# Optimization experiments

Measured on AMD Instinct MI355X. Metric: run time of the kernel, lower is better.

## Reference

```python
import jax, jax.numpy as jnp
import numpy as np
from jax.scipy.special import logsumexp

B, T, K = 256, 512, 128


def setup_inputs() -> dict:
    key = jax.random.key(0)
    k1, k2, k3, k4 = jax.random.split(key, 4)
    logits = jax.random.normal(k1, (B, T, K), dtype=jnp.float32)
    labels = jax.random.randint(k2, (B, T), 0, K)
    # lengths in [1, T] (a zero-length sequence is degenerate for a CRF)
    seq_lens = jax.random.randint(k3, (B,), 1, T + 1, dtype=jnp.int32)
    # tf.random.uniform default is U[0,1)
    trans_params = jax.random.uniform(k4, (K, K), dtype=jnp.float32)
    return {"logits": logits, "labels": labels, "seq_lens": seq_lens,
            "trans_params": trans_params}


def _viterbi_decode(logits, trans, seq_lens):
    # tfa.text.crf_decode: max-plus forward pass storing backpointers, then backtrace.
    b, t, k = logits.shape
    mask = jnp.arange(t)[None, :] < seq_lens[:, None]              # [B,T]
    alpha0 = logits[:, 0]                                           # [B,K]
    id_k = jnp.arange(k)[None, :]

    def fwd(alpha, xs):
        emit, m = xs                                                # [B,K], [B]
        scores = alpha[:, :, None] + trans[None]                    # [B,Kprev,Kcur]
        bp = jnp.where(m[:, None], jnp.argmax(scores, axis=1), id_k)
        alpha_new = jnp.where(m[:, None], jnp.max(scores, axis=1) + emit, alpha)
        return alpha_new, bp

    emits = jnp.swapaxes(logits[:, 1:], 0, 1)                       # [T-1,B,K]
    alpha_t, bps = jax.lax.scan(fwd, alpha0, (emits, mask[:, 1:].T))
    last = jnp.argmax(alpha_t, axis=1)                              # [B]

    def back(tag, bp):
        prev = jnp.take_along_axis(bp, tag[:, None], axis=1)[:, 0]
        return prev, prev

    _, tags_rev = jax.lax.scan(back, last, bps, reverse=True)       # [T-1,B]
    return jnp.concatenate([tags_rev, last[None, :]], axis=0).T     # [B,T]


def _crf_log_norm(logits, trans, seq_lens):
    # forward algorithm in log space, frozen past each sequence's length
    b, t, k = logits.shape
    mask = jnp.arange(t)[None, :] < seq_lens[:, None]

    def fwd(alpha, xs):
        emit, m = xs
        new = logsumexp(alpha[:, :, None] + trans[None], axis=1) + emit
        return jnp.where(m[:, None], new, alpha), None

    emits = jnp.swapaxes(logits[:, 1:], 0, 1)
    alpha_t, _ = jax.lax.scan(fwd, logits[:, 0], (emits, mask[:, 1:].T))
    return logsumexp(alpha_t, axis=1)                               # [B]


def _crf_sequence_score(logits, labels, trans, seq_lens):
    b, t, k = logits.shape
    mask = (jnp.arange(t)[None, :] < seq_lens[:, None]).astype(logits.dtype)
    unary = jnp.sum(jnp.take_along_axis(logits, labels[..., None], axis=2)[..., 0] * mask, axis=1)
    tmask = (jnp.arange(1, t)[None, :] < seq_lens[:, None]).astype(logits.dtype)
    binary = jnp.sum(trans[labels[:, :-1], labels[:, 1:]] * tmask, axis=1)
    return unary + binary                                           # [B]


def reference(logits, labels, seq_lens, trans_params):
    pred_ids = _viterbi_decode(logits, trans_params, seq_lens)
    log_likelihood = (_crf_sequence_score(logits, labels, trans_params, seq_lens)
                      - _crf_log_norm(logits, trans_params, seq_lens))
    loss = jnp.sum(-log_likelihood)
    return loss, pred_ids
```

## Files before the change

kernel.cpp:

```cpp
#include <hip/hip_runtime.h>
#include <math.h>

#define BB 256
#define TT 512
#define KK 128
#define AIDX(i) ((i) + (((i) >> 5) << 2))

typedef float v2f __attribute__((ext_vector_type(2)));
typedef unsigned short u16v2 __attribute__((ext_vector_type(2)));

template<int CTRL>
__device__ __forceinline__ int dpp_i(int x) {
  return __builtin_amdgcn_update_dpp(x, x, CTRL, 0xF, 0xF, true);
}
template<int CTRL>
__device__ __forceinline__ float dpp_f(float x) {
  return __int_as_float(dpp_i<CTRL>(__float_as_int(x)));
}
__device__ __forceinline__ float swz16_f(float x) {
  return __int_as_float(__builtin_amdgcn_ds_swizzle(__float_as_int(x), 0x401F));
}
__device__ __forceinline__ int pkminu16(int a, int b) {
  u16v2 av = *(u16v2*)&a, bv = *(u16v2*)&b;
  u16v2 r = __builtin_elementwise_min(av, bv);
  return *(int*)&r;
}
#define BARRIER_LGKM() asm volatile("s_waitcnt lgkmcnt(0)\ns_barrier" ::: "memory")

__global__ __launch_bounds__(512, 4) void crf_fwd(
    const float* __restrict__ logits,
    const int* __restrict__ labels,
    const int* __restrict__ seq_lens,
    const float* __restrict__ trans,
    float* __restrict__ negll,
    int* __restrict__ lastIdx,
    float* __restrict__ mOut)
{
  const int tid = threadIdx.x;
  const int cg = tid >> 3, rg = tid & 7;
  const int j0 = cg * 2, i0 = rg * 16;

  if (blockIdx.x < BB) {
    const int b = blockIdx.x;
    const int L = seq_lens[b];
    __shared__ __align__(16) float av[2][144];
    __shared__ float rv[8]; __shared__ int ri[8];

    v2f tv[16];
#pragma unroll
    for (int ii = 0; ii < 16; ++ii)
      tv[ii] = *(const v2f*)&trans[(i0 + ii) * KK + j0];

    if (tid < KK) av[0][AIDX(tid)] = logits[(b * TT) * KK + tid];

    v2f emC[4], emN[4];
#pragma unroll
    for (int s = 0; s < 4; ++s) {
      int t2 = 1 + s; if (t2 > L - 1) t2 = (L > 1) ? (L - 1) : 0;
      emC[s] = *(const v2f*)&logits[(b * TT + t2) * KK + j0];
    }
    __syncthreads();

    for (int tc = 1; tc < L; tc += 4) {
#pragma unroll
      for (int s = 0; s < 4; ++s) {
        int t2 = tc + 4 + s; if (t2 > L - 1) t2 = L - 1;
        emN[s] = *(const v2f*)&logits[(b * TT + t2) * KK + j0];
      }
#pragma unroll
      for (int s = 0; s < 4; ++s) {
        const int t = tc + s;
        if (t >= L) break;
        const float4* avr = (const float4*)(av[(t & 1) ^ 1] + AIDX(i0));
        v2f sv[16];
#pragma unroll
        for (int q = 0; q < 4; ++q) {
          float4 a4 = avr[q];
#pragma unroll
          for (int c = 0; c < 4; ++c) {
            float a = (c == 0) ? a4.x : (c == 1) ? a4.y : (c == 2) ? a4.z : a4.w;
            sv[q * 4 + c] = (v2f){a, a} + tv[q * 4 + c];
          }
        }
        v2f m;
        {
          v2f m0 = __builtin_elementwise_max(sv[0], sv[1]);
          v2f m1 = __builtin_elementwise_max(sv[2], sv[3]);
          v2f m2 = __builtin_elementwise_max(sv[4], sv[5]);
          v2f m3 = __builtin_elementwise_max(sv[6], sv[7]);
          v2f m4 = __builtin_elementwise_max(sv[8], sv[9]);
          v2f m5 = __builtin_elementwise_max(sv[10], sv[11]);
          v2f m6 = __builtin_elementwise_max(sv[12], sv[13]);
          v2f m7 = __builtin_elementwise_max(sv[14], sv[15]);
          m0 = __builtin_elementwise_max(m0, m1);
          m2 = __builtin_elementwise_max(m2, m3);
          m4 = __builtin_elementwise_max(m4, m5);
          m6 = __builtin_elementwise_max(m6, m7);
          m0 = __builtin_elementwise_max(m0, m2);
          m4 = __builtin_elementwise_max(m4, m6);
          m = __builtin_elementwise_max(m0, m4);
        }
        {
          v2f o;
          o.x = dpp_f<0xB1>(m.x); o.y = dpp_f<0xB1>(m.y);
          m = __builtin_elementwise_max(m, o);
          o.x = dpp_f<0x4E>(m.x); o.y = dpp_f<0x4E>(m.y);
          m = __builtin_elementwise_max(m, o);
          o.x = dpp_f<0x141>(m.x); o.y = dpp_f<0x141>(m.y);
          m = __builtin_elementwise_max(m, o);
        }
        v2f nav = m + emC[s];
        if (rg == 0) {
          *(v2f*)(av[t & 1] + AIDX(j0)) = nav;
          *(v2f*)&mOut[(b * TT + t) * KK + j0] = m;
        }
        BARRIER_LGKM();
      }
#pragma unroll
      for (int s = 0; s < 4; ++s) emC[s] = emN[s];
    }

    const float* avf = av[(L - 1) & 1];
    {
      float v = (tid < KK) ? avf[AIDX(tid)] : -3.4e38f;
      int idx = (tid < KK) ? tid : KK;
#pragma unroll
      for (int mm = 1; mm < 64; mm <<= 1) {
        float ov = __shfl_xor(v, mm);
        int oi = __shfl_xor(idx, mm);
        if (ov > v || (ov == v && oi < idx)) { v = ov; idx = oi; }
      }
      if ((tid & 63) == 0) { rv[tid >> 6] = v; ri[tid >> 6] = idx; }
    }
    __syncthreads();
    if (tid == 0) {
      float bv = rv[0]; int bi = ri[0];
#pragma unroll
      for (int w = 1; w < 8; ++w)
        if (rv[w] > bv || (rv[w] == bv && ri[w] < bi)) { bv = rv[w]; bi = ri[w]; }
      lastIdx[b] = bi;
    }

  } else {
    const int b = blockIdx.x - BB;
    const int L = seq_lens[b];
    __shared__ __align__(16) float ev[2][144];
    __shared__ __align__(16) float wmax[16];
    __shared__ float rs[8]; __shared__ float rsc[8];

    v2f tw[16];
#pragma unroll
    for (int ii = 0; ii < 16; ++ii) {
      v2f tr = *(const v2f*)&trans[(i0 + ii) * KK + j0];
      tw[ii].x = __expf(tr.x);
      tw[ii].y = __expf(tr.y);
    }
    if (tid < KK) ev[0][AIDX(tid)] = __expf(logits[(b * TT) * KK + tid]);
    if (tid < 16) wmax[tid] = 1.0f;

    v2f emC[4], emN[4];
#pragma unroll
    for (int s = 0; s < 4; ++s) {
      int t2 = 1 + s; if (t2 > L - 1) t2 = (L > 1) ? (L - 1) : 0;
      emC[s] = *(const v2f*)&logits[(b * TT + t2) * KK + j0];
    }
    __syncthreads();

    float Cln = 0.0f;
    for (int tc = 1; tc < L; tc += 4) {
#pragma unroll
      for (int s = 0; s < 4; ++s) {
        int t2 = tc + 4 + s; if (t2 > L - 1) t2 = L - 1;
        emN[s] = *(const v2f*)&logits[(b * TT + t2) * KK + j0];
      }
      float r;
      {
        float4 w0 = *(const float4*)&wmax[0];
        float4 w1 = *(const float4*)&wmax[4];
        float4 w2 = *(const float4*)&wmax[8];
        float4 w3 = *(const float4*)&wmax[12];
        float U = fmaxf(fmaxf(fmaxf(w0.x, w0.y), fmaxf(w0.z, w0.w)),
                        fmaxf(fmaxf(w1.x, w1.y), fmaxf(w1.z, w1.w)));
        U = fmaxf(U, fmaxf(fmaxf(fmaxf(w2.x, w2.y), fmaxf(w2.z, w2.w)),
                           fmaxf(fmaxf(w3.x, w3.y), fmaxf(w3.z, w3.w))));
        int ex = (__float_as_int(U) >> 23) & 255;
        r = __int_as_float((254 - ex) << 23);
        Cln += (float)(ex - 127) * 0.6931471805599453f;
      }
#pragma unroll
      for (int s = 0; s < 4; ++s) {
        const int t = tc + s;
        if (t >= L) break;
        const float4* evr = (const float4*)(ev[(t & 1) ^ 1] + AIDX(i0));
        v2f S2 = {0.0f, 0.0f};
#pragma unroll
        for (int q = 0; q < 4; ++q) {
          float4 e4 = evr[q];
#pragma unroll
          for (int c = 0; c < 4; ++c) {
            float e = (c == 0) ? e4.x : (c == 1) ? e4.y : (c == 2) ? e4.z : e4.w;
            S2 += (v2f){e, e} * tw[q * 4 + c];
          }
        }
        {
          v2f o;
          o.x = dpp_f<0xB1>(S2.x); o.y = dpp_f<0xB1>(S2.y); S2 += o;
          o.x = dpp_f<0x4E>(S2.x); o.y = dpp_f<0x4E>(S2.y); S2 += o;
          o.x = dpp_f<0x141>(S2.x); o.y = dpp_f<0x141>(S2.y); S2 += o;
        }
        v2f em2 = emC[s];
        float evn0 = S2.x * __expf(em2.x);
        float evn1 = S2.y * __expf(em2.y);
        if (s == 0) { evn0 *= r; evn1 *= r; }
        if (rg == 0)
          *(v2f*)(ev[t & 1] + AIDX(j0)) = (v2f){evn0, evn1};
        if (s == 3) {
          float wm = fmaxf(evn0, evn1);
          wm = fmaxf(wm, dpp_f<0x140>(wm));
          wm = fmaxf(wm, swz16_f(wm));
          if ((tid & 31) == 0) wmax[tid >> 5] = wm;
        }
        BARRIER_LGKM();
      }
#pragma unroll
      for (int s = 0; s < 4; ++s) emC[s] = emN[s];
    }

    const float* evf = ev[(L - 1) & 1];
    {
      float ssum = (tid < KK) ? evf[AIDX(tid)] : 0.0f;
#pragma unroll
      for (int mm = 1; mm < 64; mm <<= 1) ssum += __shfl_xor(ssum, mm);
      if ((tid & 63) == 0) rs[tid >> 6] = ssum;
    }
    float sc = 0.0f;
    for (int tt2 = tid; tt2 < L; tt2 += 512) {
      int lab = labels[b * TT + tt2];
      sc += logits[(b * TT + tt2) * KK + lab];
      if (tt2 >= 1) sc += trans[labels[b * TT + tt2 - 1] * KK + lab];
    }
#pragma unroll
    for (int mm = 1; mm < 64; mm <<= 1) sc += __shfl_xor(sc, mm);
    if ((tid & 63) == 0) rsc[tid >> 6] = sc;
    __syncthreads();
    if (tid == 0) {
      float es = rs[0]; float scf = rsc[0];
#pragma unroll
      for (int w = 1; w < 8; ++w) { es += rs[w]; scf += rsc[w]; }
      negll[b] = (Cln + logf(es)) - scf;
    }
  }
}

__global__ __launch_bounds__(64, 1) void crf_backtrack(
    const float* __restrict__ mvec,
    const float* __restrict__ logits,
    const int* __restrict__ seq_lens,
    const int* __restrict__ lastIdx,
    const float* __restrict__ trans,
    float* __restrict__ pred_out)
{
  const int b = blockIdx.x, l = threadIdx.x;
  const int L = seq_lens[b];
  __shared__ float tT[KK][KK + 2];
  __shared__ float tagsf[TT];

  for (int i = 0; i < KK; ++i) {
    v2f r = *(const v2f*)&trans[i * KK + 2 * l];
    tT[2 * l][i] = r.x;
    tT[2 * l + 1][i] = r.y;
  }
  const int last = lastIdx[b];
  for (int t = l; t < TT; t += 64) tagsf[t] = (float)last;
  __syncthreads();

  if (L >= 2) {
    const float* mb = mvec   + (size_t)(b * TT) * KK + 2 * l;
    const float* gb = logits + (size_t)(b * TT) * KK + 2 * l;
    int tag = last;
    v2f mvC = *(const v2f*)&mb[(size_t)(L - 1) * KK];

    v2f lg0, lg1, lg2, lg3, lg4, lg5, lg6, lg7;
    v2f mv0, mv1, mv2, mv3, mv4, mv5, mv6, mv7;
#define INITLD(P) { int s_ = L - 2 - (P); int sc_ = s_ < 0 ? 0 : s_;            \
      lg##P = *(const v2f*)&gb[(size_t)sc_ * KK];                              \
      mv##P = *(const v2f*)&mb[(size_t)sc_ * KK]; }
    INITLD(0) INITLD(1) INITLD(2) INITLD(3)
    INITLD(4) INITLD(5) INITLD(6) INITLD(7)
#undef INITLD

    int t = L - 1;

#define STEP_BODY(LG, MV, GUARDED)                                             \
    {                                                                          \
      const int tp = t - 1;                                                    \
      v2f aP;                                                                  \
      if (GUARDED) aP = (tp >= 1) ? (MV + LG) : LG;                            \
      else         aP = MV + LG;                                               \
      int lanem = tag >> 1;                                                    \
      int txi = __builtin_amdgcn_readlane(__float_as_int(mvC.x), lanem);       \
      int tyi = __builtin_amdgcn_readlane(__float_as_int(mvC.y), lanem);       \
      float target = __int_as_float((tag & 1) ? tyi : txi);                    \
      v2f col = *(const v2f*)&tT[tag][2 * l];                                  \
      v2f sv = aP + col;                           \
      bool h0 = (sv.x == target), h1 = (sv.y == target);                       \
      unsigned long long mask = __ballot(h0 || h1);                            \
      int first = __ffsll(mask) - 1;                 \
      int cand = h0 ? (2 * l) : (2 * l + 1);                                   \
      tag = __builtin_amdgcn_readlane(cand, first);                            \
      if (l == 0) tagsf[tp] = (float)tag;                                      \
      mvC = MV;                                                                \
    }

    while (t >= 9) {
#define MAIN_PHASE(P)                                                          \
      STEP_BODY(lg##P, mv##P, false)                                           \
      { int sN = t - 9; int sc_ = sN < 0 ? 0 : sN;                             \
        lg##P = *(const v2f*)&gb[(size_t)sc_ * KK];                            \
        mv##P = *(const v2f*)&mb[(size_t)sc_ * KK]; }                          \
      --t;
      MAIN_PHASE(0) MAIN_PHASE(1) MAIN_PHASE(2) MAIN_PHASE(3)
      MAIN_PHASE(4) MAIN_PHASE(5) MAIN_PHASE(6) MAIN_PHASE(7)
#undef MAIN_PHASE
    }

    while (t >= 1) {
      const int tp = t - 1;
      int sc_ = tp < 1 ? 0 : tp;
      v2f lgE = *(const v2f*)&gb[(size_t)tp * KK];
      v2f mvE = *(const v2f*)&mb[(size_t)sc_ * KK];
      STEP_BODY(lgE, mvE, true)
      --t;
    }
#undef STEP_BODY
  }
  __syncthreads();
#pragma unroll
  for (int k = 0; k < 8; ++k)
    pred_out[b * TT + l * 8 + k] = tagsf[l * 8 + k];
}

__global__ __launch_bounds__(512, 4) void crf_main_fb(
    const float* __restrict__ logits,
    const int* __restrict__ labels,
    const int* __restrict__ seq_lens,
    const float* __restrict__ trans,
    float* __restrict__ pred_out,
    float* __restrict__ negll,
    unsigned char* __restrict__ bp)
{
  const int tid = threadIdx.x;
  const int cg = tid >> 3, rg = tid & 7;
  const int j0 = cg * 2, i0 = rg * 16;

  if (blockIdx.x < BB) {
    const int b = blockIdx.x;
    const int L = seq_lens[b];
    __shared__ __align__(16) float av[2][144];
    __shared__ unsigned char tags[TT];
    __shared__ float rv[8]; __shared__ int ri[8];
    __shared__ int last_s;

    v2f tv[16];
#pragma unroll
    for (int ii = 0; ii < 16; ++ii)
      tv[ii] = *(const v2f*)&trans[(i0 + ii) * KK + j0];

    if (tid < KK) av[0][AIDX(tid)] = logits[(b * TT) * KK + tid];

    v2f emC[4], emN[4];
#pragma unroll
    for (int s = 0; s < 4; ++s) {
      int t2 = 1 + s; if (t2 > L - 1) t2 = (L > 1) ? (L - 1) : 0;
      emC[s] = *(const v2f*)&logits[(b * TT + t2) * KK + j0];
    }
    __syncthreads();

    unsigned int pw0 = 0, pw1 = 0; int pend_c = -1;

    for (int tc = 1; tc < L; tc += 4) {
#pragma unroll
      for (int s = 0; s < 4; ++s) {
        int t2 = tc + 4 + s; if (t2 > L - 1) t2 = L - 1;
        emN[s] = *(const v2f*)&logits[(b * TT + t2) * KK + j0];
      }
      if (pend_c >= 0 && rg == 1) {
        *(uint2*)(bp + (((b << 7) + pend_c) << 9) + (cg << 3)) =
            make_uint2(pw0, pw1);
      }
      unsigned int w0 = 0, w1 = 0;
#pragma unroll
      for (int s = 0; s < 4; ++s) {
        const int t = tc + s;
        if (t >= L) break;
        const float4* avr = (const float4*)(av[(t & 1) ^ 1] + AIDX(i0));
        v2f sv[16];
#pragma unroll
        for (int q = 0; q < 4; ++q) {
          float4 a4 = avr[q];
#pragma unroll
          for (int c = 0; c < 4; ++c) {
            float a = (c == 0) ? a4.x : (c == 1) ? a4.y : (c == 2) ? a4.z : a4.w;
            sv[q * 4 + c] = (v2f){a, a} + tv[q * 4 + c];
          }
        }
        v2f m;
        {
          v2f m0 = __builtin_elementwise_max(sv[0], sv[1]);
          v2f m1 = __builtin_elementwise_max(sv[2], sv[3]);
          v2f m2 = __builtin_elementwise_max(sv[4], sv[5]);
          v2f m3 = __builtin_elementwise_max(sv[6], sv[7]);
          v2f m4 = __builtin_elementwise_max(sv[8], sv[9]);
          v2f m5 = __builtin_elementwise_max(sv[10], sv[11]);
          v2f m6 = __builtin_elementwise_max(sv[12], sv[13]);
          v2f m7 = __builtin_elementwise_max(sv[14], sv[15]);
          m0 = __builtin_elementwise_max(m0, m1);
          m2 = __builtin_elementwise_max(m2, m3);
          m4 = __builtin_elementwise_max(m4, m5);
          m6 = __builtin_elementwise_max(m6, m7);
          m0 = __builtin_elementwise_max(m0, m2);
          m4 = __builtin_elementwise_max(m4, m6);
          m = __builtin_elementwise_max(m0, m4);
        }
        {
          v2f o;
          o.x = dpp_f<0xB1>(m.x); o.y = dpp_f<0xB1>(m.y);
          m = __builtin_elementwise_max(m, o);
          o.x = dpp_f<0x4E>(m.x); o.y = dpp_f<0x4E>(m.y);
          m = __builtin_elementwise_max(m, o);
          o.x = dpp_f<0x141>(m.x); o.y = dpp_f<0x141>(m.y);
          m = __builtin_elementwise_max(m, o);
        }
        int ai0 = 0xFFFF, ai1 = 0xFFFF;
#pragma unroll
        for (int i = 15; i >= 0; --i) {
          ai0 = (sv[i].x == m.x) ? (i0 + i) : ai0;
          ai1 = (sv[i].y == m.y) ? (i0 + i) : ai1;
        }
        int aip = ai0 | (ai1 << 16);
        aip = pkminu16(aip, dpp_i<0xB1>(aip));
        aip = pkminu16(aip, dpp_i<0x4E>(aip));
        aip = pkminu16(aip, dpp_i<0x141>(aip));

        v2f em2 = emC[s];
        if (rg == 0)
          *(v2f*)(av[t & 1] + AIDX(j0)) = m + em2;
        unsigned int pk = ((unsigned int)aip & 0xFFu) |
                          (((unsigned int)aip >> 8) & 0xFF00u);
        unsigned int sh = pk << ((s & 1) * 16);
        if (s < 2) w0 |= sh; else w1 |= sh;
        BARRIER_LGKM();
      }
      pw0 = w0; pw1 = w1; pend_c = (tc - 1) >> 2;
#pragma unroll
      for (int s = 0; s < 4; ++s) emC[s] = emN[s];
    }
    if (pend_c >= 0 && rg == 1) {
      *(uint2*)(bp + (((b << 7) + pend_c) << 9) + (cg << 3)) =
          make_uint2(pw0, pw1);
    }

    const float* avf = av[(L - 1) & 1];
    {
      float v = (tid < KK) ? avf[AIDX(tid)] : -3.4e38f;
      int idx = (tid < KK) ? tid : KK;
#pragma unroll
      for (int mm = 1; mm < 64; mm <<= 1) {
        float ov = __shfl_xor(v, mm);
        int oi = __shfl_xor(idx, mm);
        if (ov > v || (ov == v && oi < idx)) { v = ov; idx = oi; }
      }
      if ((tid & 63) == 0) { rv[tid >> 6] = v; ri[tid >> 6] = idx; }
    }
    __syncthreads();
    if (tid == 0) {
      float bv = rv[0]; int bi = ri[0];
#pragma unroll
      for (int w = 1; w < 8; ++w)
        if (rv[w] > bv || (rv[w] == bv && ri[w] < bi)) { bv = rv[w]; bi = ri[w]; }
      last_s = bi;
    }
    __syncthreads();
    const int last = last_s;
    if (tid >= L - 1 && tid < TT) tags[tid] = (unsigned char)last;
    __syncthreads();

    if (tid < 64 && L >= 2) {
      const uint2* bpv = (const uint2*)bp;
      int tag = last;
      int cTop = (L - 2) >> 2;
      uint2 q = bpv[(((b << 7) + cTop) << 6) + tid];
      for (int c = cTop; c >= 0; --c) {
        uint2 qn;
        if (c > 0) qn = bpv[(((b << 7) + (c - 1)) << 6) + tid];
        int sHi = (L - 2) - 4 * c; if (sHi > 3) sHi = 3;
#pragma unroll
        for (int s = 3; s >= 0; --s) {
          if (s <= sHi) {
            int word = (s < 2) ? (int)q.x : (int)q.y;
            unsigned int w = (unsigned int)__shfl(word, tag >> 1);
            tag = (int)((w >> ((((s & 1) << 1) | (tag & 1)) << 3)) & 255u);
            if (tid == 0) tags[4 * c + s] = (unsigned char)tag;
          }
        }
        q = qn;
      }
    }
    __syncthreads();
    pred_out[b * TT + tid] = (float)tags[tid];

  } else {
    const int b = blockIdx.x - BB;
    const int L = seq_lens[b];
    __shared__ __align__(16) float ev[2][144];
    __shared__ __align__(16) float wmax[16];
    __shared__ float rs[8]; __shared__ float rsc[8];

    v2f tw[16];
#pragma unroll
    for (int ii = 0; ii < 16; ++ii) {
      v2f tr = *(const v2f*)&trans[(i0 + ii) * KK + j0];
      tw[ii].x = __expf(tr.x);
      tw[ii].y = __expf(tr.y);
    }
    if (tid < KK) ev[0][AIDX(tid)] = __expf(logits[(b * TT) * KK + tid]);
    if (tid < 16) wmax[tid] = 1.0f;

    v2f emC[4], emN[4];
#pragma unroll
    for (int s = 0; s < 4; ++s) {
      int t2 = 1 + s; if (t2 > L - 1) t2 = (L > 1) ? (L - 1) : 0;
      emC[s] = *(const v2f*)&logits[(b * TT + t2) * KK + j0];
    }
    __syncthreads();

    float Cln = 0.0f;
    for (int tc = 1; tc < L; tc += 4) {
#pragma unroll
      for (int s = 0; s < 4; ++s) {
        int t2 = tc + 4 + s; if (t2 > L - 1) t2 = L - 1;
        emN[s] = *(const v2f*)&logits[(b * TT + t2) * KK + j0];
      }
      float r;
      {
        float4 w0 = *(const float4*)&wmax[0];
        float4 w1 = *(const float4*)&wmax[4];
        float4 w2 = *(const float4*)&wmax[8];
        float4 w3 = *(const float4*)&wmax[12];
        float U = fmaxf(fmaxf(fmaxf(w0.x, w0.y), fmaxf(w0.z, w0.w)),
                        fmaxf(fmaxf(w1.x, w1.y), fmaxf(w1.z, w1.w)));
        U = fmaxf(U, fmaxf(fmaxf(fmaxf(w2.x, w2.y), fmaxf(w2.z, w2.w)),
                           fmaxf(fmaxf(w3.x, w3.y), fmaxf(w3.z, w3.w))));
        int ex = (__float_as_int(U) >> 23) & 255;
        r = __int_as_float((254 - ex) << 23);
        Cln += (float)(ex - 127) * 0.6931471805599453f;
      }
#pragma unroll
      for (int s = 0; s < 4; ++s) {
        const int t = tc + s;
        if (t >= L) break;
        const float4* evr = (const float4*)(ev[(t & 1) ^ 1] + AIDX(i0));
        v2f S2 = {0.0f, 0.0f};
#pragma unroll
        for (int q = 0; q < 4; ++q) {
          float4 e4 = evr[q];
#pragma unroll
          for (int c = 0; c < 4; ++c) {
            float e = (c == 0) ? e4.x : (c == 1) ? e4.y : (c == 2) ? e4.z : e4.w;
            S2 += (v2f){e, e} * tw[q * 4 + c];
          }
        }
        {
          v2f o;
          o.x = dpp_f<0xB1>(S2.x); o.y = dpp_f<0xB1>(S2.y); S2 += o;
          o.x = dpp_f<0x4E>(S2.x); o.y = dpp_f<0x4E>(S2.y); S2 += o;
          o.x = dpp_f<0x141>(S2.x); o.y = dpp_f<0x141>(S2.y); S2 += o;
        }
        v2f em2 = emC[s];
        float evn0 = S2.x * __expf(em2.x);
        float evn1 = S2.y * __expf(em2.y);
        if (s == 0) { evn0 *= r; evn1 *= r; }
        if (rg == 0)
          *(v2f*)(ev[t & 1] + AIDX(j0)) = (v2f){evn0, evn1};
        if (s == 3) {
          float wm = fmaxf(evn0, evn1);
          wm = fmaxf(wm, dpp_f<0x140>(wm));
          wm = fmaxf(wm, swz16_f(wm));
          if ((tid & 31) == 0) wmax[tid >> 5] = wm;
        }
        BARRIER_LGKM();
      }
#pragma unroll
      for (int s = 0; s < 4; ++s) emC[s] = emN[s];
    }

    const float* evf = ev[(L - 1) & 1];
    {
      float ssum = (tid < KK) ? evf[AIDX(tid)] : 0.0f;
#pragma unroll
      for (int mm = 1; mm < 64; mm <<= 1) ssum += __shfl_xor(ssum, mm);
      if ((tid & 63) == 0) rs[tid >> 6] = ssum;
    }
    float sc = 0.0f;
    for (int tt2 = tid; tt2 < L; tt2 += 512) {
      int lab = labels[b * TT + tt2];
      sc += logits[(b * TT + tt2) * KK + lab];
      if (tt2 >= 1) sc += trans[labels[b * TT + tt2 - 1] * KK + lab];
    }
#pragma unroll
    for (int mm = 1; mm < 64; mm <<= 1) sc += __shfl_xor(sc, mm);
    if ((tid & 63) == 0) rsc[tid >> 6] = sc;
    __syncthreads();
    if (tid == 0) {
      float es = rs[0]; float scf = rsc[0];
#pragma unroll
      for (int w = 1; w < 8; ++w) { es += rs[w]; scf += rsc[w]; }
      negll[b] = (Cln + logf(es)) - scf;
    }
  }
}

__global__ void crf_loss_reduce(const float* __restrict__ negll, float* __restrict__ out) {
  int tid = threadIdx.x;
  float v = negll[tid];
#pragma unroll
  for (int m = 1; m < 64; m <<= 1) v += __shfl_xor(v, m);
  __shared__ float p[4];
  if ((tid & 63) == 0) p[tid >> 6] = v;
  __syncthreads();
  if (tid == 0) out[0] = p[0] + p[1] + p[2] + p[3];
}

extern "C" void kernel_launch(void* const* d_in, const int* in_sizes, int n_in,
                              void* d_out, int out_size, void* d_ws, size_t ws_size,
                              hipStream_t stream) {
  const float* logits   = (const float*)d_in[0];
  const int*   labels   = (const int*)d_in[1];
  const int*   seq_lens = (const int*)d_in[2];
  const float* trans    = (const float*)d_in[3];
  float* out = (float*)d_out;

  float* negll = (float*)d_ws;
  const size_t M_OFF = 4096;
  const size_t NEED = M_OFF + (size_t)BB * TT * KK * 4;

  if (ws_size >= NEED) {
    int*   lastIdx = (int*)((char*)d_ws + 1024);
    float* mOut    = (float*)((char*)d_ws + M_OFF);
    crf_fwd<<<2 * BB, 512, 0, stream>>>(logits, labels, seq_lens, trans,
                                        negll, lastIdx, mOut);
    crf_backtrack<<<BB, 64, 0, stream>>>(mOut, logits, seq_lens, lastIdx,
                                         trans, out + 1);
  } else {
    unsigned char* bp = (unsigned char*)d_ws + 1024;
    crf_main_fb<<<2 * BB, 512, 0, stream>>>(logits, labels, seq_lens, trans,
                                            out + 1, negll, bp);
  }
  crf_loss_reduce<<<1, 256, 0, stream>>>(negll, out);
}
```

Baseline: 435.3 us.

## Fuse Viterbi backtrack into the forward kernel's Viterbi blocks

The separate backtrack kernel is removed. Each Viterbi block of the forward kernel now runs the backtrace itself with one wavefront, after staging the transposed transition matrix and a tag buffer in a shared-memory arena that is carved up by offsets. This removes a kernel launch and its serialization, and lets backtraces for short sequences overlap with the log-norm blocks still running. The cost is more LDS per block (about 70KB), which can limit how many blocks fit per CU, and 448 idle threads sitting in each block during the serial backtrace.

```diff
diff --git a/kernel.cpp b/kernel.cpp
--- a/kernel.cpp
+++ b/kernel.cpp
@@ -6,6 +6,17 @@
 #define KK 128
 #define AIDX(i) ((i) + (((i) >> 5) << 2))
 
+#define SM_TT    0
+#define SM_AV    16640
+#define SM_TAGS  16928
+#define SM_RV    17440
+#define SM_RI    17448
+#define SM_LAST  17456
+#define SM_WMAX  17460
+#define SM_RS    17476
+#define SM_RSC   17484
+#define SM_TOTAL 17496
+
 typedef float v2f __attribute__((ext_vector_type(2)));
 typedef unsigned short u16v2 __attribute__((ext_vector_type(2)));
 
@@ -27,15 +38,16 @@
 }
 #define BARRIER_LGKM() asm volatile("s_waitcnt lgkmcnt(0)\ns_barrier" ::: "memory")
 
-__global__ __launch_bounds__(512, 4) void crf_fwd(
+__global__ __launch_bounds__(512, 4) void crf_main(
     const float* __restrict__ logits,
     const int* __restrict__ labels,
     const int* __restrict__ seq_lens,
     const float* __restrict__ trans,
+    float* __restrict__ pred_out,
     float* __restrict__ negll,
-    int* __restrict__ lastIdx,
     float* __restrict__ mOut)
 {
+  __shared__ __align__(16) float smem[SM_TOTAL];
   const int tid = threadIdx.x;
   const int cg = tid >> 3, rg = tid & 7;
   const int j0 = cg * 2, i0 = rg * 16;
@@ -43,8 +55,17 @@
   if (blockIdx.x < BB) {
     const int b = blockIdx.x;
     const int L = seq_lens[b];
-    __shared__ __align__(16) float av[2][144];
-    __shared__ float rv[8]; __shared__ int ri[8];
+    float* tT    = smem + SM_TT;
+    float (*av)[144] = (float(*)[144])(smem + SM_AV);
+    float* tagsf = smem + SM_TAGS;
+    float* rv    = smem + SM_RV;
+    int*   ri    = (int*)(smem + SM_RI);
+    int*   last_s = (int*)(smem + SM_LAST);
+
+    for (int e = tid; e < KK * KK; e += 512) {
+      int i = e >> 7, j = e & 127;
+      tT[j * 130 + i] = trans[e];
+    }
 
     v2f tv[16];
 #pragma unroll
@@ -138,15 +159,87 @@
 #pragma unroll
       for (int w = 1; w < 8; ++w)
         if (rv[w] > bv || (rv[w] == bv && ri[w] < bi)) { bv = rv[w]; bi = ri[w]; }
-      lastIdx[b] = bi;
-    }
+      *last_s = bi;
+    }
+    __syncthreads();
+    const int last = *last_s;
+    for (int t = tid; t < TT; t += 512) tagsf[t] = (float)last;
+    __syncthreads();
+
+    if (tid >= 64) return;
+    const int l = tid;
+
+    if (L >= 2) {
+      const float* mb = mOut   + (size_t)(b * TT) * KK + 2 * l;
+      const float* gb = logits + (size_t)(b * TT) * KK + 2 * l;
+      int tag = last;
+      v2f mvC = *(const v2f*)&mb[(size_t)(L - 1) * KK];
+
+      v2f lg0, lg1, lg2, lg3, lg4, lg5, lg6, lg7;
+      v2f mv0, mv1, mv2, mv3, mv4, mv5, mv6, mv7;
+#define INITLD(P) { int s_ = L - 2 - (P); int sc_ = s_ < 0 ? 0 : s_;           \
+      lg##P = *(const v2f*)&gb[(size_t)sc_ * KK];                              \
+      mv##P = *(const v2f*)&mb[(size_t)sc_ * KK]; }
+      INITLD(0) INITLD(1) INITLD(2) INITLD(3)
+      INITLD(4) INITLD(5) INITLD(6) INITLD(7)
+#undef INITLD
+
+      int t = L - 1;
+
+#define STEP_BODY(LG, MV, GUARDED)                                             \
+      {                                                                        \
+        const int tp = t - 1;                                                  \
+        v2f aP;                                                                \
+        if (GUARDED) aP = (tp >= 1) ? (MV + LG) : LG;                          \
+        else         aP = MV + LG;                                             \
+        int lanem = tag >> 1;                                                  \
+        int txi = __builtin_amdgcn_readlane(__float_as_int(mvC.x), lanem);     \
+        int tyi = __builtin_amdgcn_readlane(__float_as_int(mvC.y), lanem);     \
+        float target = __int_as_float((tag & 1) ? tyi : txi);                  \
+        v2f col = *(const v2f*)&tT[tag * 130 + 2 * l];                         \
+        v2f sv = aP + col;                         \
+        bool h0 = (sv.x == target), h1 = (sv.y == target);                     \
+        unsigned long long mask = __ballot(h0 || h1);                          \
+        int first = __ffsll(mask) - 1;               \
+        int cand = h0 ? (2 * l) : (2 * l + 1);                                 \
+        tag = __builtin_amdgcn_readlane(cand, first);                          \
+        if (l == 0) tagsf[tp] = (float)tag;                                    \
+        mvC = MV;                                                              \
+      }
+
+      while (t >= 9) {
+#define MAIN_PHASE(P)                                                          \
+        STEP_BODY(lg##P, mv##P, false)                                         \
+        { int sN = t - 9; int sc_ = sN < 0 ? 0 : sN;                           \
+          lg##P = *(const v2f*)&gb[(size_t)sc_ * KK];                          \
+          mv##P = *(const v2f*)&mb[(size_t)sc_ * KK]; }                        \
+        --t;
+        MAIN_PHASE(0) MAIN_PHASE(1) MAIN_PHASE(2) MAIN_PHASE(3)
+        MAIN_PHASE(4) MAIN_PHASE(5) MAIN_PHASE(6) MAIN_PHASE(7)
+#undef MAIN_PHASE
+      }
+
+      while (t >= 1) {
+        const int tp = t - 1;
+        int sc_ = tp < 1 ? 0 : tp;
+        v2f lgE = *(const v2f*)&gb[(size_t)tp * KK];
+        v2f mvE = *(const v2f*)&mb[(size_t)sc_ * KK];
+        STEP_BODY(lgE, mvE, true)
+        --t;
+      }
+#undef STEP_BODY
+    }
+#pragma unroll
+    for (int k = 0; k < 8; ++k)
+      pred_out[b * TT + l * 8 + k] = tagsf[l * 8 + k];
 
   } else {
     const int b = blockIdx.x - BB;
     const int L = seq_lens[b];
-    __shared__ __align__(16) float ev[2][144];
-    __shared__ __align__(16) float wmax[16];
-    __shared__ float rs[8]; __shared__ float rsc[8];
+    float (*ev)[144] = (float(*)[144])(smem + SM_AV);
+    float* wmax = smem + SM_WMAX;
+    float* rs   = smem + SM_RS;
+    float* rsc  = smem + SM_RSC;
 
     v2f tw[16];
 #pragma unroll
@@ -250,94 +343,6 @@
       negll[b] = (Cln + logf(es)) - scf;
     }
   }
-}
-
-__global__ __launch_bounds__(64, 1) void crf_backtrack(
-    const float* __restrict__ mvec,
-    const float* __restrict__ logits,
-    const int* __restrict__ seq_lens,
-    const int* __restrict__ lastIdx,
-    const float* __restrict__ trans,
-    float* __restrict__ pred_out)
-{
-  const int b = blockIdx.x, l = threadIdx.x;
-  const int L = seq_lens[b];
-  __shared__ float tT[KK][KK + 2];
-  __shared__ float tagsf[TT];
-
-  for (int i = 0; i < KK; ++i) {
-    v2f r = *(const v2f*)&trans[i * KK + 2 * l];
-    tT[2 * l][i] = r.x;
-    tT[2 * l + 1][i] = r.y;
-  }
-  const int last = lastIdx[b];
-  for (int t = l; t < TT; t += 64) tagsf[t] = (float)last;
-  __syncthreads();
-
-  if (L >= 2) {
-    const float* mb = mvec   + (size_t)(b * TT) * KK + 2 * l;
-    const float* gb = logits + (size_t)(b * TT) * KK + 2 * l;
-    int tag = last;
-    v2f mvC = *(const v2f*)&mb[(size_t)(L - 1) * KK];
-
-    v2f lg0, lg1, lg2, lg3, lg4, lg5, lg6, lg7;
-    v2f mv0, mv1, mv2, mv3, mv4, mv5, mv6, mv7;
-#define INITLD(P) { int s_ = L - 2 - (P); int sc_ = s_ < 0 ? 0 : s_;            \
-      lg##P = *(const v2f*)&gb[(size_t)sc_ * KK];                              \
-      mv##P = *(const v2f*)&mb[(size_t)sc_ * KK]; }
-    INITLD(0) INITLD(1) INITLD(2) INITLD(3)
-    INITLD(4) INITLD(5) INITLD(6) INITLD(7)
-#undef INITLD
-
-    int t = L - 1;
-
-#define STEP_BODY(LG, MV, GUARDED)                                             \
-    {                                                                          \
-      const int tp = t - 1;                                                    \
-      v2f aP;                                                                  \
-      if (GUARDED) aP = (tp >= 1) ? (MV + LG) : LG;                            \
-      else         aP = MV + LG;                                               \
-      int lanem = tag >> 1;                                                    \
-      int txi = __builtin_amdgcn_readlane(__float_as_int(mvC.x), lanem);       \
-      int tyi = __builtin_amdgcn_readlane(__float_as_int(mvC.y), lanem);       \
-      float target = __int_as_float((tag & 1) ? tyi : txi);                    \
-      v2f col = *(const v2f*)&tT[tag][2 * l];                                  \
-      v2f sv = aP + col;                           \
-      bool h0 = (sv.x == target), h1 = (sv.y == target);                       \
-      unsigned long long mask = __ballot(h0 || h1);                            \
-      int first = __ffsll(mask) - 1;                 \
-      int cand = h0 ? (2 * l) : (2 * l + 1);                                   \
-      tag = __builtin_amdgcn_readlane(cand, first);                            \
-      if (l == 0) tagsf[tp] = (float)tag;                                      \
-      mvC = MV;                                                                \
-    }
-
-    while (t >= 9) {
-#define MAIN_PHASE(P)                                                          \
-      STEP_BODY(lg##P, mv##P, false)                                           \
-      { int sN = t - 9; int sc_ = sN < 0 ? 0 : sN;                             \
-        lg##P = *(const v2f*)&gb[(size_t)sc_ * KK];                            \
-        mv##P = *(const v2f*)&mb[(size_t)sc_ * KK]; }                          \
-      --t;
-      MAIN_PHASE(0) MAIN_PHASE(1) MAIN_PHASE(2) MAIN_PHASE(3)
-      MAIN_PHASE(4) MAIN_PHASE(5) MAIN_PHASE(6) MAIN_PHASE(7)
-#undef MAIN_PHASE
-    }
-
-    while (t >= 1) {
-      const int tp = t - 1;
-      int sc_ = tp < 1 ? 0 : tp;
-      v2f lgE = *(const v2f*)&gb[(size_t)tp * KK];
-      v2f mvE = *(const v2f*)&mb[(size_t)sc_ * KK];
-      STEP_BODY(lgE, mvE, true)
-      --t;
-    }
-#undef STEP_BODY
-  }
-  __syncthreads();
-#pragma unroll
-  for (int k = 0; k < 8; ++k)
-    pred_out[b * TT + l * 8 + k] = tagsf[l * 8 + k];
 }
 
 __global__ __launch_bounds__(512, 4) void crf_main_fb(
@@ -645,12 +650,9 @@
   const size_t NEED = M_OFF + (size_t)BB * TT * KK * 4;
 
   if (ws_size >= NEED) {
-    int*   lastIdx = (int*)((char*)d_ws + 1024);
-    float* mOut    = (float*)((char*)d_ws + M_OFF);
-    crf_fwd<<<2 * BB, 512, 0, stream>>>(logits, labels, seq_lens, trans,
-                                        negll, lastIdx, mOut);
-    crf_backtrack<<<BB, 64, 0, stream>>>(mOut, logits, seq_lens, lastIdx,
-                                         trans, out + 1);
+    float* mOut = (float*)((char*)d_ws + M_OFF);
+    crf_main<<<2 * BB, 512, 0, stream>>>(logits, labels, seq_lens, trans,
+                                         out + 1, negll, mOut);
   } else {
     unsigned char* bp = (unsigned char*)d_ws + 1024;
     crf_main_fb<<<2 * BB, 512, 0, stream>>>(logits, labels, seq_lens, trans,
```

After: 379.4 us, median of 2. 1.15x faster.

## Merge Viterbi, forward-algorithm and backtrack into one 1024-thread block per sequence

Applied to the files above, without the earlier changes.

Fuses the two-kernel path (a forward kernel with separate Viterbi and log-norm blocks, then a backtrack kernel) into a single kernel. Each block of 1024 threads handles one sequence: the first 512 threads run the Viterbi max-plus recursion and the other 512 run the scaled forward algorithm, sharing barriers. The block then does the backtrack in its first wavefront using a transposed trans matrix in LDS. This removes a kernel launch and the global round-trip of lastIdx, but couples the two recursions to one barrier schedule. It also leaves most of the 1024-thread block idle during the serial backtrack, which reduces how much backtrack work can overlap with other blocks' recursions.

```diff
diff --git a/kernel.cpp b/kernel.cpp
--- a/kernel.cpp
+++ b/kernel.cpp
@@ -6,6 +6,18 @@
 #define KK 128
 #define AIDX(i) ((i) + (((i) >> 5) << 2))
 
+#define SM_TT    0
+#define SM_AV    16640
+#define SM_EV    16928
+#define SM_TAGS  17216
+#define SM_WMAX  17728
+#define SM_RV    17744
+#define SM_RI    17752
+#define SM_RS    17760
+#define SM_RSC   17768
+#define SM_LAST  17776
+#define SM_TOTAL 17780
+
 typedef float v2f __attribute__((ext_vector_type(2)));
 typedef unsigned short u16v2 __attribute__((ext_vector_type(2)));
 
@@ -27,50 +39,90 @@
 }
 #define BARRIER_LGKM() asm volatile("s_waitcnt lgkmcnt(0)\ns_barrier" ::: "memory")
 
-__global__ __launch_bounds__(512, 4) void crf_fwd(
+__global__ __launch_bounds__(1024, 4) void crf_merged(
     const float* __restrict__ logits,
     const int* __restrict__ labels,
     const int* __restrict__ seq_lens,
     const float* __restrict__ trans,
+    float* __restrict__ pred_out,
     float* __restrict__ negll,
-    int* __restrict__ lastIdx,
     float* __restrict__ mOut)
 {
+  __shared__ __align__(16) float smem[SM_TOTAL];
   const int tid = threadIdx.x;
-  const int cg = tid >> 3, rg = tid & 7;
+  const bool isV = tid < 512;
+  const int ht = isV ? tid : tid - 512;
+  const int cg = ht >> 3, rg = ht & 7;
   const int j0 = cg * 2, i0 = rg * 16;
-
-  if (blockIdx.x < BB) {
-    const int b = blockIdx.x;
-    const int L = seq_lens[b];
-    __shared__ __align__(16) float av[2][144];
-    __shared__ float rv[8]; __shared__ int ri[8];
-
-    v2f tv[16];
+  const int b = blockIdx.x;
+  const int L = seq_lens[b];
+
+  float* tT    = smem + SM_TT;
+  float (*av)[144] = (float(*)[144])(smem + SM_AV);
+  float (*ev)[144] = (float(*)[144])(smem + SM_EV);
+  float* tagsf = smem + SM_TAGS;
+  float* wmax  = smem + SM_WMAX;
+  float* rv    = smem + SM_RV;
+  int*   ri    = (int*)(smem + SM_RI);
+  float* rs    = smem + SM_RS;
+  float* rsc   = smem + SM_RSC;
+  int*   last_s = (int*)(smem + SM_LAST);
+
+  v2f tA[16];
+  if (isV) {
+    for (int e = ht; e < KK * KK; e += 512) {
+      int i = e >> 7, j = e & 127;
+      tT[j * 130 + i] = trans[e];
+    }
 #pragma unroll
     for (int ii = 0; ii < 16; ++ii)
-      tv[ii] = *(const v2f*)&trans[(i0 + ii) * KK + j0];
-
-    if (tid < KK) av[0][AIDX(tid)] = logits[(b * TT) * KK + tid];
-
-    v2f emC[4], emN[4];
+      tA[ii] = *(const v2f*)&trans[(i0 + ii) * KK + j0];
+    if (ht < KK) av[0][AIDX(ht)] = logits[(b * TT) * KK + ht];
+  } else {
+#pragma unroll
+    for (int ii = 0; ii < 16; ++ii) {
+      v2f tr = *(const v2f*)&trans[(i0 + ii) * KK + j0];
+      tA[ii].x = __expf(tr.x);
+      tA[ii].y = __expf(tr.y);
+    }
+    if (ht < KK) ev[0][AIDX(ht)] = __expf(logits[(b * TT) * KK + ht]);
+    if (ht < 16) wmax[ht] = 1.0f;
+  }
+
+  v2f emC[4], emN[4];
+#pragma unroll
+  for (int s = 0; s < 4; ++s) {
+    int t2 = 1 + s; if (t2 > L - 1) t2 = (L > 1) ? (L - 1) : 0;
+    emC[s] = *(const v2f*)&logits[(b * TT + t2) * KK + j0];
+  }
+  __syncthreads();
+
+  float Cln = 0.0f;
+  for (int tc = 1; tc < L; tc += 4) {
 #pragma unroll
     for (int s = 0; s < 4; ++s) {
-      int t2 = 1 + s; if (t2 > L - 1) t2 = (L > 1) ? (L - 1) : 0;
-      emC[s] = *(const v2f*)&logits[(b * TT + t2) * KK + j0];
-    }
-    __syncthreads();
-
-    for (int tc = 1; tc < L; tc += 4) {
-#pragma unroll
-      for (int s = 0; s < 4; ++s) {
-        int t2 = tc + 4 + s; if (t2 > L - 1) t2 = L - 1;
-        emN[s] = *(const v2f*)&logits[(b * TT + t2) * KK + j0];
-      }
-#pragma unroll
-      for (int s = 0; s < 4; ++s) {
-        const int t = tc + s;
-        if (t >= L) break;
+      int t2 = tc + 4 + s; if (t2 > L - 1) t2 = L - 1;
+      emN[s] = *(const v2f*)&logits[(b * TT + t2) * KK + j0];
+    }
+    float r = 0.0f;
+    if (!isV) {
+      float4 w0 = *(const float4*)&wmax[0];
+      float4 w1 = *(const float4*)&wmax[4];
+      float4 w2 = *(const float4*)&wmax[8];
+      float4 w3 = *(const float4*)&wmax[12];
+      float U = fmaxf(fmaxf(fmaxf(w0.x, w0.y), fmaxf(w0.z, w0.w)),
+                      fmaxf(fmaxf(w1.x, w1.y), fmaxf(w1.z, w1.w)));
+      U = fmaxf(U, fmaxf(fmaxf(fmaxf(w2.x, w2.y), fmaxf(w2.z, w2.w)),
+                         fmaxf(fmaxf(w3.x, w3.y), fmaxf(w3.z, w3.w))));
+      int ex = (__float_as_int(U) >> 23) & 255;
+      r = __int_as_float((254 - ex) << 23);
+      Cln += (float)(ex - 127) * 0.6931471805599453f;
+    }
+#pragma unroll
+    for (int s = 0; s < 4; ++s) {
+      const int t = tc + s;
+      if (t >= L) break;
+      if (isV) {
         const float4* avr = (const float4*)(av[(t & 1) ^ 1] + AIDX(i0));
         v2f sv[16];
 #pragma unroll
@@ -79,7 +131,7 @@
 #pragma unroll
           for (int c = 0; c < 4; ++c) {
             float a = (c == 0) ? a4.x : (c == 1) ? a4.y : (c == 2) ? a4.z : a4.w;
-            sv[q * 4 + c] = (v2f){a, a} + tv[q * 4 + c];
+            sv[q * 4 + c] = (v2f){a, a} + tA[q * 4 + c];
           }
         }
         v2f m;
@@ -114,83 +166,7 @@
           *(v2f*)(av[t & 1] + AIDX(j0)) = nav;
           *(v2f*)&mOut[(b * TT + t) * KK + j0] = m;
         }
-        BARRIER_LGKM();
-      }
-#pragma unroll
-      for (int s = 0; s < 4; ++s) emC[s] = emN[s];
-    }
-
-    const float* avf = av[(L - 1) & 1];
-    {
-      float v = (tid < KK) ? avf[AIDX(tid)] : -3.4e38f;
-      int idx = (tid < KK) ? tid : KK;
-#pragma unroll
-      for (int mm = 1; mm < 64; mm <<= 1) {
-        float ov = __shfl_xor(v, mm);
-        int oi = __shfl_xor(idx, mm);
-        if (ov > v || (ov == v && oi < idx)) { v = ov; idx = oi; }
-      }
-      if ((tid & 63) == 0) { rv[tid >> 6] = v; ri[tid >> 6] = idx; }
-    }
-    __syncthreads();
-    if (tid == 0) {
-      float bv = rv[0]; int bi = ri[0];
-#pragma unroll
-      for (int w = 1; w < 8; ++w)
-        if (rv[w] > bv || (rv[w] == bv && ri[w] < bi)) { bv = rv[w]; bi = ri[w]; }
-      lastIdx[b] = bi;
-    }
-
-  } else {
-    const int b = blockIdx.x - BB;
-    const int L = seq_lens[b];
-    __shared__ __align__(16) float ev[2][144];
-    __shared__ __align__(16) float wmax[16];
-    __shared__ float rs[8]; __shared__ float rsc[8];
-
-    v2f tw[16];
-#pragma unroll
-    for (int ii = 0; ii < 16; ++ii) {
-      v2f tr = *(const v2f*)&trans[(i0 + ii) * KK + j0];
-      tw[ii].x = __expf(tr.x);
-      tw[ii].y = __expf(tr.y);
-    }
-    if (tid < KK) ev[0][AIDX(tid)] = __expf(logits[(b * TT) * KK + tid]);
-    if (tid < 16) wmax[tid] = 1.0f;
-
-    v2f emC[4], emN[4];
-#pragma unroll
-    for (int s = 0; s < 4; ++s) {
-      int t2 = 1 + s; if (t2 > L - 1) t2 = (L > 1) ? (L - 1) : 0;
-      emC[s] = *(const v2f*)&logits[(b * TT + t2) * KK + j0];
-    }
-    __syncthreads();
-
-    float Cln = 0.0f;
-    for (int tc = 1; tc < L; tc += 4) {
-#pragma unroll
-      for (int s = 0; s < 4; ++s) {
-        int t2 = tc + 4 + s; if (t2 > L - 1) t2 = L - 1;
-        emN[s] = *(const v2f*)&logits[(b * TT + t2) * KK + j0];
-      }
-      float r;
-      {
-        float4 w0 = *(const float4*)&wmax[0];
-        float4 w1 = *(const float4*)&wmax[4];
-        float4 w2 = *(const float4*)&wmax[8];
-        float4 w3 = *(const float4*)&wmax[12];
-        float U = fmaxf(fmaxf(fmaxf(w0.x, w0.y), fmaxf(w0.z, w0.w)),
-                        fmaxf(fmaxf(w1.x, w1.y), fmaxf(w1.z, w1.w)));
-        U = fmaxf(U, fmaxf(fmaxf(fmaxf(w2.x, w2.y), fmaxf(w2.z, w2.w)),
-                           fmaxf(fmaxf(w3.x, w3.y), fmaxf(w3.z, w3.w))));
-        int ex = (__float_as_int(U) >> 23) & 255;
-        r = __int_as_float((254 - ex) << 23);
-        Cln += (float)(ex - 127) * 0.6931471805599453f;
-      }
-#pragma unroll
-      for (int s = 0; s < 4; ++s) {
-        const int t = tc + s;
-        if (t >= L) break;
+      } else {
         const float4* evr = (const float4*)(ev[(t & 1) ^ 1] + AIDX(i0));
         v2f S2 = {0.0f, 0.0f};
 #pragma unroll
@@ -199,7 +175,7 @@
 #pragma unroll
           for (int c = 0; c < 4; ++c) {
             float e = (c == 0) ? e4.x : (c == 1) ? e4.y : (c == 2) ? e4.z : e4.w;
-            S2 += (v2f){e, e} * tw[q * 4 + c];
+            S2 += (v2f){e, e} * tA[q * 4 + c];
           }
         }
         {
@@ -218,73 +194,75 @@
           float wm = fmaxf(evn0, evn1);
           wm = fmaxf(wm, dpp_f<0x140>(wm));
           wm = fmaxf(wm, swz16_f(wm));
-          if ((tid & 31) == 0) wmax[tid >> 5] = wm;
-        }
-        BARRIER_LGKM();
-      }
-#pragma unroll
-      for (int s = 0; s < 4; ++s) emC[s] = emN[s];
-    }
-
+          if ((ht & 31) == 0) wmax[ht >> 5] = wm;
+        }
+      }
+      BARRIER_LGKM();
+    }
+#pragma unroll
+    for (int s = 0; s < 4; ++s) emC[s] = emN[s];
+  }
+
+  if (isV) {
+    const float* avf = av[(L - 1) & 1];
+    float v = (ht < KK) ? avf[AIDX(ht)] : -3.4e38f;
+    int idx = (ht < KK) ? ht : KK;
+#pragma unroll
+    for (int mm = 1; mm < 64; mm <<= 1) {
+      float ov = __shfl_xor(v, mm);
+      int oi = __shfl_xor(idx, mm);
+      if (ov > v || (ov == v && oi < idx)) { v = ov; idx = oi; }
+    }
+    if ((ht & 63) == 0) { rv[ht >> 6] = v; ri[ht >> 6] = idx; }
+  } else {
     const float* evf = ev[(L - 1) & 1];
-    {
-      float ssum = (tid < KK) ? evf[AIDX(tid)] : 0.0f;
-#pragma unroll
-      for (int mm = 1; mm < 64; mm <<= 1) ssum += __shfl_xor(ssum, mm);
-      if ((tid & 63) == 0) rs[tid >> 6] = ssum;
-    }
+    float ssum = (ht < KK) ? evf[AIDX(ht)] : 0.0f;
+#pragma unroll
+    for (int mm = 1; mm < 64; mm <<= 1) ssum += __shfl_xor(ssum, mm);
+    if ((ht & 63) == 0) rs[ht >> 6] = ssum;
     float sc = 0.0f;
-    for (int tt2 = tid; tt2 < L; tt2 += 512) {
+    for (int tt2 = ht; tt2 < L; tt2 += 512) {
       int lab = labels[b * TT + tt2];
       sc += logits[(b * TT + tt2) * KK + lab];
       if (tt2 >= 1) sc += trans[labels[b * TT + tt2 - 1] * KK + lab];
     }
 #pragma unroll
     for (int mm = 1; mm < 64; mm <<= 1) sc += __shfl_xor(sc, mm);
-    if ((tid & 63) == 0) rsc[tid >> 6] = sc;
-    __syncthreads();
-    if (tid == 0) {
-      float es = rs[0]; float scf = rsc[0];
-#pragma unroll
-      for (int w = 1; w < 8; ++w) { es += rs[w]; scf += rsc[w]; }
-      negll[b] = (Cln + logf(es)) - scf;
-    }
-  }
-}
-
-__global__ __launch_bounds__(64, 1) void crf_backtrack(
-    const float* __restrict__ mvec,
-    const float* __restrict__ logits,
-    const int* __restrict__ seq_lens,
-    const int* __restrict__ lastIdx,
-    const float* __restrict__ trans,
-    float* __restrict__ pred_out)
-{
-  const int b = blockIdx.x, l = threadIdx.x;
-  const int L = seq_lens[b];
-  __shared__ float tT[KK][KK + 2];
-  __shared__ float tagsf[TT];
-
-  for (int i = 0; i < KK; ++i) {
-    v2f r = *(const v2f*)&trans[i * KK + 2 * l];
-    tT[2 * l][i] = r.x;
-    tT[2 * l + 1][i] = r.y;
-  }
-  const int last = lastIdx[b];
-  for (int t = l; t < TT; t += 64) tagsf[t] = (float)last;
+    if ((ht & 63) == 0) rsc[ht >> 6] = sc;
+  }
   __syncthreads();
+  if (tid == 0) {
+    float bv = rv[0]; int bi = ri[0];
+#pragma unroll
+    for (int w = 1; w < 8; ++w)
+      if (rv[w] > bv || (rv[w] == bv && ri[w] < bi)) { bv = rv[w]; bi = ri[w]; }
+    *last_s = bi;
+  }
+  if (tid == 512) {
+    float es = rs[0]; float scf = rsc[0];
+#pragma unroll
+    for (int w = 1; w < 8; ++w) { es += rs[w]; scf += rsc[w]; }
+    negll[b] = (Cln + logf(es)) - scf;
+  }
+  __syncthreads();
+  const int last = *last_s;
+  if (tid < TT) tagsf[tid] = (float)last;
+  __syncthreads();
+
+  if (tid >= 64) return;
+  const int l = tid;
 
   if (L >= 2) {
-    const float* mb = mvec   + (size_t)(b * TT) * KK + 2 * l;
+    const float* mb = mOut   + (size_t)(b * TT) * KK + 2 * l;
     const float* gb = logits + (size_t)(b * TT) * KK + 2 * l;
     int tag = last;
     v2f mvC = *(const v2f*)&mb[(size_t)(L - 1) * KK];
 
     v2f lg0, lg1, lg2, lg3, lg4, lg5, lg6, lg7;
     v2f mv0, mv1, mv2, mv3, mv4, mv5, mv6, mv7;
-#define INITLD(P) { int s_ = L - 2 - (P); int sc_ = s_ < 0 ? 0 : s_;            \
-      lg##P = *(const v2f*)&gb[(size_t)sc_ * KK];                              \
-      mv##P = *(const v2f*)&mb[(size_t)sc_ * KK]; }
+#define INITLD(P) { int s_ = L - 2 - (P); int sc_ = s_ < 0 ? 0 : s_;           \
+    lg##P = *(const v2f*)&gb[(size_t)sc_ * KK];                                \
+    mv##P = *(const v2f*)&mb[(size_t)sc_ * KK]; }
     INITLD(0) INITLD(1) INITLD(2) INITLD(3)
     INITLD(4) INITLD(5) INITLD(6) INITLD(7)
 #undef INITLD
@@ -301,7 +279,7 @@
       int txi = __builtin_amdgcn_readlane(__float_as_int(mvC.x), lanem);       \
       int tyi = __builtin_amdgcn_readlane(__float_as_int(mvC.y), lanem);       \
       float target = __int_as_float((tag & 1) ? tyi : txi);                    \
-      v2f col = *(const v2f*)&tT[tag][2 * l];                                  \
+      v2f col = *(const v2f*)&tT[tag * 130 + 2 * l];                           \
       v2f sv = aP + col;                           \
       bool h0 = (sv.x == target), h1 = (sv.y == target);                       \
       unsigned long long mask = __ballot(h0 || h1);                            \
@@ -323,7 +301,6 @@
       MAIN_PHASE(4) MAIN_PHASE(5) MAIN_PHASE(6) MAIN_PHASE(7)
 #undef MAIN_PHASE
     }
-
     while (t >= 1) {
       const int tp = t - 1;
       int sc_ = tp < 1 ? 0 : tp;
@@ -334,7 +311,6 @@
     }
 #undef STEP_BODY
   }
-  __syncthreads();
 #pragma unroll
   for (int k = 0; k < 8; ++k)
     pred_out[b * TT + l * 8 + k] = tagsf[l * 8 + k];
@@ -645,12 +621,9 @@
   const size_t NEED = M_OFF + (size_t)BB * TT * KK * 4;
 
   if (ws_size >= NEED) {
-    int*   lastIdx = (int*)((char*)d_ws + 1024);
-    float* mOut    = (float*)((char*)d_ws + M_OFF);
-    crf_fwd<<<2 * BB, 512, 0, stream>>>(logits, labels, seq_lens, trans,
-                                        negll, lastIdx, mOut);
-    crf_backtrack<<<BB, 64, 0, stream>>>(mOut, logits, seq_lens, lastIdx,
-                                         trans, out + 1);
+    float* mOut = (float*)((char*)d_ws + M_OFF);
+    crf_merged<<<BB, 1024, 0, stream>>>(logits, labels, seq_lens, trans,
+                                        out + 1, negll, mOut);
   } else {
     unsigned char* bp = (unsigned char*)d_ws + 1024;
     crf_main_fb<<<2 * BB, 512, 0, stream>>>(logits, labels, seq_lens, trans,
```

After: 463.4 us. 6.5% more time.
